# Performance work log

Hardware: AMD Instinct MI355X
Metric: run time of the kernel (lower is better)

The kernel has to match this reference:

```python
import jax, jax.numpy as jnp
import numpy as np

N_HEAD = 16

def setup_inputs() -> dict:
    key = jax.random.key(0)
    k1, k2 = jax.random.split(key)
    B, T, C = 4, 2048, 1024
    x = jax.random.normal(k1, (B, T, C), dtype=jnp.float32)
    # fused QKV projection weight, stored as [C, 3C] so qkv = x @ w_qkv
    # (equivalent to torch Linear(C, 3C, bias=False) with weight.T)
    w_qkv = jax.random.normal(k2, (C, 3 * C), dtype=jnp.float32) * (1.0 / np.sqrt(C))
    return {"x": x, "w_qkv": w_qkv}

def reference(x, w_qkv):
    B, T, C = x.shape
    H = N_HEAD
    D = C // H
    qkv = x @ w_qkv                                  # [B, T, 3C]
    q, k, v = jnp.split(qkv, 3, axis=2)              # each [B, T, C]
    q = q.reshape(B, T, H, D).transpose(0, 2, 1, 3)  # [B, H, T, D]
    k = k.reshape(B, T, H, D).transpose(0, 2, 1, 3)
    v = v.reshape(B, T, H, D).transpose(0, 2, 1, 3)
    scale = np.float32(1.0 / np.sqrt(D))
    att = jnp.einsum('bhqd,bhkd->bhqk', q, k) * scale   # [B, H, T, T]
    causal = jnp.tril(jnp.ones((T, T), dtype=bool))     # lower-tri = visible
    att = jnp.where(causal, att, -jnp.inf)
    att = jax.nn.softmax(att, axis=-1)
    out = jnp.einsum('bhqk,bhkd->bhqd', att, v)          # [B, H, T, D]
    return out.transpose(0, 2, 1, 3).reshape(B, T, C)
```

## Files before the change

### kernel.cpp

```cpp
#include <hip/hip_runtime.h>


#define B_ 4
#define T_ 2048
#define C_ 1024
#define H_ 16
#define D_ 64
#define QKV1 (B_*H_*T_*D_)

typedef __attribute__((ext_vector_type(4))) float  f32x4;
typedef __attribute__((ext_vector_type(8))) short  bf16x8;
typedef __attribute__((ext_vector_type(4))) short  bf16x4;

__device__ inline unsigned short f2bf(float f) {
  unsigned int u = __builtin_bit_cast(unsigned int, f);
  u += 0x7FFFu + ((u >> 16) & 1u);
  return (unsigned short)(u >> 16);
}

__device__ inline void gload16(const unsigned short* g, unsigned short* l) {
  __builtin_amdgcn_global_load_lds(
      (const __attribute__((address_space(1))) void*)g,
      (__attribute__((address_space(3))) void*)l, 16, 0, 0);
}

__global__ __launch_bounds__(256) void convert_x(const float* __restrict__ x,
                                                 unsigned short* __restrict__ xb) {
  size_t i = ((size_t)blockIdx.x * 256 + threadIdx.x) * 16;
  f32x4 a = *(const f32x4*)(x + i);
  f32x4 b = *(const f32x4*)(x + i + 4);
  f32x4 c = *(const f32x4*)(x + i + 8);
  f32x4 d = *(const f32x4*)(x + i + 12);
  bf16x8 o0, o1;
#pragma unroll
  for (int j = 0; j < 4; j++) {
    o0[j]     = (short)f2bf(a[j]);
    o0[j + 4] = (short)f2bf(b[j]);
    o1[j]     = (short)f2bf(c[j]);
    o1[j + 4] = (short)f2bf(d[j]);
  }
  *(bf16x8*)(xb + i) = o0;
  *(bf16x8*)(xb + i + 8) = o1;
}

__global__ __launch_bounds__(256) void transpose_w(const float* __restrict__ w,
                                                   unsigned short* __restrict__ wt) {
  __shared__ float tile[32][33];
  const int tx = threadIdx.x & 31, ty = threadIdx.x >> 5;
  const int n0 = blockIdx.x * 32, k0 = blockIdx.y * 32;
#pragma unroll
  for (int j = 0; j < 4; j++) {
    int k = ty + j * 8;
    tile[k][tx] = w[(size_t)(k0 + k) * 3072 + n0 + tx];
  }
  __syncthreads();
#pragma unroll
  for (int j = 0; j < 4; j++) {
    int n = ty + j * 8;
    wt[(size_t)(n0 + n) * 1024 + k0 + tx] = f2bf(tile[tx][n]);
  }
}

__global__ __launch_bounds__(256) void qkv_gemm(const unsigned short* __restrict__ xb,
                                                const unsigned short* __restrict__ wt,
                                                unsigned short* __restrict__ qkv) {
  __shared__ unsigned short Al[128 * 64];
  __shared__ unsigned short Bl[128 * 64];
  const int tid = threadIdx.x;
  const int lane = tid & 63, wid = tid >> 6;
  const int l15 = lane & 15, g = lane >> 4;
  const int m0 = blockIdx.y * 128, n0 = blockIdx.x * 128;
  const int wm = (wid >> 1) * 64, wn = (wid & 1) * 64;

  f32x4 acc[4][4] = {};

  const int srow[4] = { (0 * 256 + tid) >> 3, (1 * 256 + tid) >> 3,
                        (2 * 256 + tid) >> 3, (3 * 256 + tid) >> 3 };
  int scol[4];
#pragma unroll
  for (int sw = 0; sw < 4; sw++) {
    int s = sw * 256 + tid;
    scol[sw] = (s & 7) ^ (srow[sw] & 7);
  }

  for (int k0 = 0; k0 < 1024; k0 += 64) {
    __syncthreads();
#pragma unroll
    for (int sw = 0; sw < 4; sw++) {
      unsigned short* ldsA = &Al[(sw * 256 + wid * 64) * 8];
      unsigned short* ldsB = &Bl[(sw * 256 + wid * 64) * 8];
      gload16(xb + (size_t)(m0 + srow[sw]) * 1024 + k0 + scol[sw] * 8, ldsA);
      gload16(wt + (size_t)(n0 + srow[sw]) * 1024 + k0 + scol[sw] * 8, ldsB);
    }
    __syncthreads();

#pragma unroll
    for (int ks = 0; ks < 2; ks++) {
      bf16x8 af[4], bfr[4];
#pragma unroll
      for (int mt = 0; mt < 4; mt++) {
        int row = wm + mt * 16 + l15;
        int c = (ks * 4 + g) ^ (row & 7);
        af[mt] = *(const bf16x8*)&Al[(row * 8 + c) * 8];
      }
#pragma unroll
      for (int nt = 0; nt < 4; nt++) {
        int row = wn + nt * 16 + l15;
        int c = (ks * 4 + g) ^ (row & 7);
        bfr[nt] = *(const bf16x8*)&Bl[(row * 8 + c) * 8];
      }
#pragma unroll
      for (int mt = 0; mt < 4; mt++)
#pragma unroll
        for (int nt = 0; nt < 4; nt++)
          acc[mt][nt] = __builtin_amdgcn_mfma_f32_16x16x32_bf16(af[mt], bfr[nt], acc[mt][nt], 0, 0, 0);
    }
  }

  const int r0 = g * 4, cc = l15;
#pragma unroll
  for (int mt = 0; mt < 4; mt++)
#pragma unroll
    for (int nt = 0; nt < 4; nt++)
#pragma unroll
      for (int r = 0; r < 4; r++) {
        int m = m0 + wm + mt * 16 + r0 + r;
        int n = n0 + wn + nt * 16 + cc;
        int b = m >> 11, t = m & 2047;
        int which = n >> 10, c = n & 1023;
        int h = c >> 6, d = c & 63;
        qkv[(size_t)which * QKV1 + ((size_t)((b * H_ + h) * T_ + t)) * D_ + d] =
            f2bf(acc[mt][nt][r]);
      }
}

__global__ __launch_bounds__(256, 4) void attn(const unsigned short* __restrict__ qkv,
                                               float* __restrict__ out) {
  __shared__ unsigned short Kl[64][72];
  __shared__ unsigned short Vl[64][72];
  __shared__ unsigned short Pl[4][16][72];
  const int tid = threadIdx.x, lane = tid & 63, wq = tid >> 6;
  const int l15 = lane & 15, g = lane >> 4;
  const int bh = blockIdx.y;
  const int xp = blockIdx.x;
  const int qta = xp, qtb = 31 - xp;
  const int ntiles = qtb + 1;
  const size_t base = (size_t)bh * (T_ * D_);
  const unsigned short* qp = qkv + base;
  const unsigned short* kp = qkv + (size_t)QKV1 + base;
  const unsigned short* vp = qkv + 2 * (size_t)QKV1 + base;

  bf16x8 qfa[2], qfb[2];
#define LOADQ(QF, Q0)                                                          \
  do {                                                                         \
    int qrow_ = (Q0) + wq * 16 + l15;                                          \
    _Pragma("unroll")                                                          \
    for (int kc = 0; kc < 2; kc++) {                                           \
      bf16x8 v = *(const bf16x8*)(qp + (size_t)qrow_ * 64 + kc * 32 + g * 8);  \
      _Pragma("unroll")                                                        \
      for (int j = 0; j < 8; j++) {                                            \
        unsigned short u = (unsigned short)v[j];                               \
        int e = u & 0x7F80;                                                    \
        u = (e > (3 << 7)) ? (unsigned short)(u - (3 << 7))                    \
                           : (unsigned short)(u & 0x8000);                     \
        v[j] = (short)u;                                                       \
      }                                                                        \
      QF[kc] = v;                                                              \
    }                                                                          \
  } while (0)
  LOADQ(qfa, qta * 64);
  LOADQ(qfb, qtb * 64);

  f32x4 oa[4] = {}, ob[4] = {};
  float rsa[4] = {0.f, 0.f, 0.f, 0.f}, rsb[4] = {0.f, 0.f, 0.f, 0.f};

  bf16x8 kreg0, kreg1, vreg0, vreg1;
  const int krow = tid >> 3, kch = tid & 7;
  const int vpr = tid >> 3, vdch = tid & 7;
#define LOADKV(IT)                                                             \
  do {                                                                         \
    size_t k0_ = (size_t)(IT) * 64;                                            \
    kreg0 = *(const bf16x8*)(kp + (k0_ + krow) * 64 + kch * 8);                \
    kreg1 = *(const bf16x8*)(kp + (k0_ + 32 + krow) * 64 + kch * 8);           \
    vreg0 = *(const bf16x8*)(vp + (k0_ + 2 * vpr) * 64 + vdch * 8);            \
    vreg1 = *(const bf16x8*)(vp + (k0_ + 2 * vpr + 1) * 64 + vdch * 8);        \
  } while (0)

#define PROCESS(QF, OACC, RS, Q0, DIAG, K0)                                    \
  do {                                                                         \
    f32x4 s_[4];                                                               \
    _Pragma("unroll")                                                          \
    for (int nt = 0; nt < 4; nt++) {                                           \
      f32x4 a_ = {0.f, 0.f, 0.f, 0.f};                                         \
      _Pragma("unroll")                                                        \
      for (int kc = 0; kc < 2; kc++) {                                         \
        bf16x8 kf = *(const bf16x8*)&Kl[nt * 16 + l15][kc * 32 + g * 8];       \
        a_ = __builtin_amdgcn_mfma_f32_16x16x32_bf16(QF[kc], kf, a_, 0, 0, 0); \
      }                                                                        \
      s_[nt] = a_;                                                             \
    }                                                                          \
    if (DIAG) {                                                                \
      _Pragma("unroll")                                                        \
      for (int nt = 0; nt < 4; nt++) {                                         \
        int kg_ = (K0) + nt * 16 + l15;                                        \
        _Pragma("unroll")                                                      \
        for (int r = 0; r < 4; r++)                                            \
          if (kg_ > (Q0) + wq * 16 + g * 4 + r) s_[nt][r] = -1e30f;            \
      }                                                                        \
    }                                                                          \
    _Pragma("unroll")                                                          \
    for (int nt = 0; nt < 4; nt++)                                             \
      _Pragma("unroll")                                                        \
      for (int r = 0; r < 4; r++) {                                            \
        float p_ = __expf(s_[nt][r]);                                          \
        RS[r] += p_;                                                           \
        Pl[wq][g * 4 + r][nt * 16 + l15] = f2bf(p_);                           \
      }                                                                        \
    asm volatile("s_waitcnt lgkmcnt(0)" ::: "memory");                         \
    bf16x8 pf0 = *(const bf16x8*)&Pl[wq][l15][g * 8];                          \
    bf16x8 pf1 = *(const bf16x8*)&Pl[wq][l15][32 + g * 8];                     \
    _Pragma("unroll")                                                          \
    for (int dt = 0; dt < 4; dt++) {                                           \
      int d_ = dt * 16 + l15;                                                  \
      int sw_ = (d_ >> 3) << 3;                                                \
      bf16x8 vf0 = *(const bf16x8*)&Vl[d_][(g * 8) ^ sw_];                     \
      bf16x8 vf1 = *(const bf16x8*)&Vl[d_][(32 + g * 8) ^ sw_];                \
      OACC[dt] = __builtin_amdgcn_mfma_f32_16x16x32_bf16(pf0, vf0, OACC[dt], 0, 0, 0); \
      OACC[dt] = __builtin_amdgcn_mfma_f32_16x16x32_bf16(pf1, vf1, OACC[dt], 0, 0, 0); \
    }                                                                          \
  } while (0)

  LOADKV(0);
  for (int it = 0; it < ntiles; ++it) {
    __syncthreads();
    *(bf16x8*)&Kl[krow][kch * 8] = kreg0;
    *(bf16x8*)&Kl[32 + krow][kch * 8] = kreg1;
#pragma unroll
    for (int j = 0; j < 8; j++) {
      int d = vdch * 8 + j;
      unsigned int pk = ((unsigned int)(unsigned short)vreg1[j] << 16) |
                        (unsigned int)(unsigned short)vreg0[j];
      *(unsigned int*)&Vl[d][(2 * vpr) ^ ((d >> 3) << 3)] = pk;
    }
    if (it + 1 < ntiles) LOADKV(it + 1);
    __syncthreads();

    PROCESS(qfb, ob, rsb, qtb * 64, it == qtb, it * 64);
    if (it <= qta) PROCESS(qfa, oa, rsa, qta * 64, it == qta, it * 64);
  }

  const int b = bh >> 4, h = bh & 15;
#define EPILOG(OACC, RS, Q0)                                                   \
  do {                                                                         \
    _Pragma("unroll")                                                          \
    for (int r = 0; r < 4; r++) {                                              \
      float t_ = RS[r];                                                        \
      t_ += __shfl_xor(t_, 1); t_ += __shfl_xor(t_, 2);                        \
      t_ += __shfl_xor(t_, 4); t_ += __shfl_xor(t_, 8);                        \
      float inv_ = 1.0f / t_;                                                  \
      int qg_ = (Q0) + wq * 16 + g * 4 + r;                                    \
      _Pragma("unroll")                                                        \
      for (int dt = 0; dt < 4; dt++)                                           \
        out[((size_t)(b * T_ + qg_)) * C_ + h * 64 + dt * 16 + l15] =          \
            OACC[dt][r] * inv_;                                                \
    }                                                                          \
  } while (0)
  EPILOG(ob, rsb, qtb * 64);
  EPILOG(oa, rsa, qta * 64);
}

extern "C" void kernel_launch(void* const* d_in, const int* in_sizes, int n_in,
                              void* d_out, int out_size, void* d_ws, size_t ws_size,
                              hipStream_t stream) {
  const float* x = (const float*)d_in[0];
  const float* w = (const float*)d_in[1];
  float* out = (float*)d_out;
  unsigned short* wt  = (unsigned short*)d_ws;
  unsigned short* qkv = wt + (size_t)3072 * 1024;
  unsigned short* xb  = (unsigned short*)d_out;

  convert_x  <<<2048, 256, 0, stream>>>(x, xb);
  transpose_w<<<dim3(96, 32), 256, 0, stream>>>(w, wt);
  qkv_gemm   <<<dim3(24, 64), 256, 0, stream>>>(xb, wt, qkv);
  attn       <<<dim3(16, 64), 256, 0, stream>>>(qkv, out);
}
```

Baseline: 153.9 us.

## Interleave both query tiles' MFMAs to share K/V LDS fragment loads

The attention loop now runs the QK^T products for both query tiles (the early and the late one) in a single pass, reusing each K fragment read from LDS for both. It does the same for the PV products, reusing each V fragment. The P staging buffer is doubled so both softmax outputs can sit in LDS at once. The MFMA blocks are wrapped in s_setprio and launch bounds drop from 4 to 3 blocks per SIMD to allow more registers, which trades occupancy for fewer LDS reads and more independent MFMA chains.

```diff
diff --git a/kernel.cpp b/kernel.cpp
--- a/kernel.cpp
+++ b/kernel.cpp
@@ -134,11 +134,11 @@
       }
 }
 
-__global__ __launch_bounds__(256, 4) void attn(const unsigned short* __restrict__ qkv,
+__global__ __launch_bounds__(256, 3) void attn(const unsigned short* __restrict__ qkv,
                                                float* __restrict__ out) {
   __shared__ unsigned short Kl[64][72];
   __shared__ unsigned short Vl[64][72];
-  __shared__ unsigned short Pl[4][16][72];
+  __shared__ unsigned short Pl[2][4][16][72];
   const int tid = threadIdx.x, lane = tid & 63, wq = tid >> 6;
   const int l15 = lane & 15, g = lane >> 4;
   const int bh = blockIdx.y;
@@ -186,48 +186,25 @@
     vreg1 = *(const bf16x8*)(vp + (k0_ + 2 * vpr + 1) * 64 + vdch * 8);        \
   } while (0)
 
-#define PROCESS(QF, OACC, RS, Q0, DIAG, K0)                                    \
+#define SOFTMAX(S, RS, PBUF, Q0, ISDIAG, K0)                                   \
   do {                                                                         \
-    f32x4 s_[4];                                                               \
-    _Pragma("unroll")                                                          \
-    for (int nt = 0; nt < 4; nt++) {                                           \
-      f32x4 a_ = {0.f, 0.f, 0.f, 0.f};                                         \
-      _Pragma("unroll")                                                        \
-      for (int kc = 0; kc < 2; kc++) {                                         \
-        bf16x8 kf = *(const bf16x8*)&Kl[nt * 16 + l15][kc * 32 + g * 8];       \
-        a_ = __builtin_amdgcn_mfma_f32_16x16x32_bf16(QF[kc], kf, a_, 0, 0, 0); \
-      }                                                                        \
-      s_[nt] = a_;                                                             \
-    }                                                                          \
-    if (DIAG) {                                                                \
+    if (ISDIAG) {                                                              \
       _Pragma("unroll")                                                        \
       for (int nt = 0; nt < 4; nt++) {                                         \
         int kg_ = (K0) + nt * 16 + l15;                                        \
         _Pragma("unroll")                                                      \
         for (int r = 0; r < 4; r++)                                            \
-          if (kg_ > (Q0) + wq * 16 + g * 4 + r) s_[nt][r] = -1e30f;            \
+          if (kg_ > (Q0) + wq * 16 + g * 4 + r) S[nt][r] = -1e30f;             \
       }                                                                        \
     }                                                                          \
     _Pragma("unroll")                                                          \
     for (int nt = 0; nt < 4; nt++)                                             \
       _Pragma("unroll")                                                        \
       for (int r = 0; r < 4; r++) {                                            \
-        float p_ = __expf(s_[nt][r]);                                          \
+        float p_ = __expf(S[nt][r]);                                           \
         RS[r] += p_;                                                           \
-        Pl[wq][g * 4 + r][nt * 16 + l15] = f2bf(p_);                           \
+        Pl[PBUF][wq][g * 4 + r][nt * 16 + l15] = f2bf(p_);                     \
       }                                                                        \
-    asm volatile("s_waitcnt lgkmcnt(0)" ::: "memory");                         \
-    bf16x8 pf0 = *(const bf16x8*)&Pl[wq][l15][g * 8];                          \
-    bf16x8 pf1 = *(const bf16x8*)&Pl[wq][l15][32 + g * 8];                     \
-    _Pragma("unroll")                                                          \
-    for (int dt = 0; dt < 4; dt++) {                                           \
-      int d_ = dt * 16 + l15;                                                  \
-      int sw_ = (d_ >> 3) << 3;                                                \
-      bf16x8 vf0 = *(const bf16x8*)&Vl[d_][(g * 8) ^ sw_];                     \
-      bf16x8 vf1 = *(const bf16x8*)&Vl[d_][(32 + g * 8) ^ sw_];                \
-      OACC[dt] = __builtin_amdgcn_mfma_f32_16x16x32_bf16(pf0, vf0, OACC[dt], 0, 0, 0); \
-      OACC[dt] = __builtin_amdgcn_mfma_f32_16x16x32_bf16(pf1, vf1, OACC[dt], 0, 0, 0); \
-    }                                                                          \
   } while (0)
 
   LOADKV(0);
@@ -245,8 +222,54 @@
     if (it + 1 < ntiles) LOADKV(it + 1);
     __syncthreads();
 
-    PROCESS(qfb, ob, rsb, qtb * 64, it == qtb, it * 64);
-    if (it <= qta) PROCESS(qfa, oa, rsa, qta * 64, it == qta, it * 64);
+    const bool doA = (it <= qta);
+
+    f32x4 sb[4], sa[4];
+    __builtin_amdgcn_s_setprio(1);
+#pragma unroll
+    for (int nt = 0; nt < 4; nt++) {
+      bf16x8 kf0 = *(const bf16x8*)&Kl[nt * 16 + l15][g * 8];
+      bf16x8 kf1 = *(const bf16x8*)&Kl[nt * 16 + l15][32 + g * 8];
+      f32x4 t0 = {0.f, 0.f, 0.f, 0.f};
+      t0 = __builtin_amdgcn_mfma_f32_16x16x32_bf16(qfb[0], kf0, t0, 0, 0, 0);
+      t0 = __builtin_amdgcn_mfma_f32_16x16x32_bf16(qfb[1], kf1, t0, 0, 0, 0);
+      sb[nt] = t0;
+      if (doA) {
+        f32x4 t1 = {0.f, 0.f, 0.f, 0.f};
+        t1 = __builtin_amdgcn_mfma_f32_16x16x32_bf16(qfa[0], kf0, t1, 0, 0, 0);
+        t1 = __builtin_amdgcn_mfma_f32_16x16x32_bf16(qfa[1], kf1, t1, 0, 0, 0);
+        sa[nt] = t1;
+      }
+    }
+    __builtin_amdgcn_s_setprio(0);
+
+    SOFTMAX(sb, rsb, 0, qtb * 64, it == qtb, it * 64);
+    if (doA) SOFTMAX(sa, rsa, 1, qta * 64, it == qta, it * 64);
+
+    asm volatile("s_waitcnt lgkmcnt(0)" ::: "memory");
+    bf16x8 pb0 = *(const bf16x8*)&Pl[0][wq][l15][g * 8];
+    bf16x8 pb1 = *(const bf16x8*)&Pl[0][wq][l15][32 + g * 8];
+    bf16x8 pa0, pa1;
+    if (doA) {
+      pa0 = *(const bf16x8*)&Pl[1][wq][l15][g * 8];
+      pa1 = *(const bf16x8*)&Pl[1][wq][l15][32 + g * 8];
+    }
+
+    __builtin_amdgcn_s_setprio(1);
+#pragma unroll
+    for (int dt = 0; dt < 4; dt++) {
+      int d_ = dt * 16 + l15;
+      int sw_ = (d_ >> 3) << 3;
+      bf16x8 vf0 = *(const bf16x8*)&Vl[d_][(g * 8) ^ sw_];
+      bf16x8 vf1 = *(const bf16x8*)&Vl[d_][(32 + g * 8) ^ sw_];
+      ob[dt] = __builtin_amdgcn_mfma_f32_16x16x32_bf16(pb0, vf0, ob[dt], 0, 0, 0);
+      ob[dt] = __builtin_amdgcn_mfma_f32_16x16x32_bf16(pb1, vf1, ob[dt], 0, 0, 0);
+      if (doA) {
+        oa[dt] = __builtin_amdgcn_mfma_f32_16x16x32_bf16(pa0, vf0, oa[dt], 0, 0, 0);
+        oa[dt] = __builtin_amdgcn_mfma_f32_16x16x32_bf16(pa1, vf1, oa[dt], 0, 0, 0);
+      }
+    }
+    __builtin_amdgcn_s_setprio(0);
   }
 
   const int b = bh >> 4, h = bh & 15;
```

New measurement: 153.5 us. Within noise of the previous version (-0.3%).
